# Performance work log

Hardware: AMD Instinct MI355X
Metric: run time of the kernel (lower is better)

The kernel has to match this reference:

```python
import jax, jax.numpy as jnp
import numpy as np
from jax import lax

E = 30      # embedding_dim
NH = 3      # attention heads
HD = E // NH
EPS = 1e-5


def _layer_norm(x, g, b):
    mu = jnp.mean(x, axis=-1, keepdims=True)
    var = jnp.mean(jnp.square(x - mu), axis=-1, keepdims=True)
    return (x - mu) * lax.rsqrt(var + EPS) * g + b


def setup_inputs() -> dict:
    key = jax.random.key(0)
    ks = jax.random.split(key, 16)
    B, T = 4096, 512
    s = 0.1  # param init scale
    return {
        "input": jax.random.normal(ks[0], (B, T, 5), jnp.float32),
        "w_ih": jax.random.normal(ks[1], (4 * E, 5), jnp.float32) * s,
        "w_hh": jax.random.normal(ks[2], (4 * E, E), jnp.float32) * s,
        "b_ih": jax.random.normal(ks[3], (4 * E,), jnp.float32) * s,
        "b_hh": jax.random.normal(ks[4], (4 * E,), jnp.float32) * s,
        "in_proj_w": jax.random.normal(ks[5], (3 * E, E), jnp.float32) * s,
        "in_proj_b": jax.random.normal(ks[6], (3 * E,), jnp.float32) * s,
        "out_proj_w": jax.random.normal(ks[7], (E, E), jnp.float32) * s,
        "out_proj_b": jax.random.normal(ks[8], (E,), jnp.float32) * s,
        "fc1_w": jax.random.normal(ks[9], (E, E), jnp.float32) * s,
        "fc1_b": jax.random.normal(ks[10], (E,), jnp.float32) * s,
        "fc2_w": jax.random.normal(ks[11], (E, E), jnp.float32) * s,
        "fc2_b": jax.random.normal(ks[12], (E,), jnp.float32) * s,
        "ln_g": jnp.ones((E,), jnp.float32),
        "ln_b": jnp.zeros((E,), jnp.float32),
        "out_w": jax.random.normal(ks[13], (3, E), jnp.float32) * s,
        "out_b": jax.random.normal(ks[14], (3,), jnp.float32) * s,
    }


def reference(input, w_ih, w_hh, b_ih, b_hh, in_proj_w, in_proj_b,
              out_proj_w, out_proj_b, fc1_w, fc1_b, fc2_w, fc2_b,
              ln_g, ln_b, out_w, out_b):
    B = input.shape[0]
    # --- LSTM (1 layer, batch_first); gate order i,f,g,o as in torch ---
    x_proj = jnp.einsum('bti,gi->btg', input, w_ih) + b_ih + b_hh  # [B,T,4E]

    def step(carry, xg):
        h, c = carry
        gates = xg + h @ w_hh.T
        i, f, g, o = jnp.split(gates, 4, axis=-1)
        i = jax.nn.sigmoid(i); f = jax.nn.sigmoid(f)
        g = jnp.tanh(g); o = jax.nn.sigmoid(o)
        c = f * c + i * g
        h = o * jnp.tanh(c)
        return (h, c), None

    h0 = jnp.zeros((B, E), input.dtype)
    (h_n, c_n), _ = lax.scan(step, (h0, h0), x_proj.transpose(1, 0, 2))

    # --- MultiheadAttention on 2D inputs: torch treats [B,E] as unbatched
    # sequences of length B, so attention mixes across the batch axis. ---
    q = h_n @ in_proj_w[:E].T + in_proj_b[:E]
    k = c_n @ in_proj_w[E:2 * E].T + in_proj_b[E:2 * E]
    v = c_n @ in_proj_w[2 * E:].T + in_proj_b[2 * E:]
    qh = q.reshape(B, NH, HD).transpose(1, 0, 2)  # [NH, B, HD]
    kh = k.reshape(B, NH, HD).transpose(1, 0, 2)
    vh = v.reshape(B, NH, HD).transpose(1, 0, 2)
    scores = jnp.einsum('hld,hmd->hlm', qh, kh) / np.sqrt(HD)  # [NH,B,B]
    attn = jax.nn.softmax(scores, axis=-1)
    ctx = jnp.einsum('hlm,hmd->hld', attn, vh)  # [NH,B,HD]
    attn_out = ctx.transpose(1, 0, 2).reshape(B, E) @ out_proj_w.T + out_proj_b

    # --- residual + shared LayerNorm + MLP (exact GELU) ---
    x1 = _layer_norm(attn_out + h_n, ln_g, ln_b)
    fc = jax.nn.gelu(x1 @ fc1_w.T + fc1_b, approximate=False) @ fc2_w.T + fc2_b
    x2 = _layer_norm(x1 + fc, ln_g, ln_b)
    return x2 @ out_w.T + out_b  # [B, 3]
```

## Files before the change

kernel.cpp:

```cpp
#include <hip/hip_runtime.h>
#include <math.h>

#define Bsz  4096
#define Tlen 512
#define NE   30
#define NIN  5
#define HD10 10
#define B10  (Bsz*HD10)

typedef _Float16 h2v  __attribute__((ext_vector_type(2)));
typedef _Float16 f16x8 __attribute__((ext_vector_type(8)));
typedef float    f32x4 __attribute__((ext_vector_type(4)));

__device__ __forceinline__ float fexp2(float x){ return __builtin_amdgcn_exp2f(x); }
__device__ __forceinline__ float frcp (float x){ return __builtin_amdgcn_rcpf(x); }
#define L2E 1.4426950408889634f

__device__ __forceinline__ void loadarr32(float arr[32], const float* bufrow){
  const float4* p4 = (const float4*)bufrow;
  #pragma unroll
  for (int q4=0;q4<8;q4++){ float4 vv=p4[q4]; arr[4*q4]=vv.x; arr[4*q4+1]=vv.y; arr[4*q4+2]=vv.z; arr[4*q4+3]=vv.w; }
}

#define XSTR 520

extern "C" __global__ void __launch_bounds__(512,1)
lstm_k(const float* __restrict__ input, const float* __restrict__ w_ih,
       const float* __restrict__ w_hh, const float* __restrict__ b_ih,
       const float* __restrict__ b_hh, const float* __restrict__ in_proj_w,
       const float* __restrict__ in_proj_b,
       float* __restrict__ qo, float* __restrict__ ko, float* __restrict__ vo,
       float* __restrict__ ho)
{
  __shared__ __align__(16) _Float16 hb[2*640];
  __shared__ __align__(16) _Float16 xh[16*XSTR];
  const int tid  = threadIdx.x;
  const int wv   = __builtin_amdgcn_readfirstlane(tid >> 6);
  const int lane = tid & 63;
  const int n    = lane & 15;
  const int quad = lane >> 4;
  const int b0   = blockIdx.x * 16;

  f16x8 ah, ax;
  f32x4 bi;
  {
    const int r  = n & 3;
    const int qm = n >> 2;
    const int dA = 8*qm + wv;
    const float sG = (r==2) ? (-2.f*L2E) : (-L2E);
    const bool rv = (dA < NE);
    const int grow = rv ? (r*NE + dA) : 0;
    #pragma unroll
    for (int j=0;j<8;++j){
      const int k = quad*8 + j;
      ah[j] = (rv && k < NE) ? (_Float16)(sG*w_hh[grow*NE + k]) : (_Float16)0;
      ax[j] = (rv && quad==0 && j < NIN) ? (_Float16)(sG*w_ih[grow*NIN + j]) : (_Float16)0;
    }
    const int d = 8*quad + wv;
    #pragma unroll
    for (int rr=0;rr<4;++rr){
      const float sR = (rr==2) ? (-2.f*L2E) : (-L2E);
      bi[rr] = (d < NE) ? sR*(b_ih[rr*NE+d] + b_hh[rr*NE+d]) : 0.f;
    }
  }
  for (int i=tid; i<640; i+=512) ((float*)hb)[i] = 0.f;
  for (int i=tid; i<16*XSTR; i+=512) xh[i] = (_Float16)0;
  __syncthreads();

  float cc=0.f, hh=0.f;
  const int rdo  = n*40 + 8*quad;
  const int wro  = n*40 + 8*quad + wv;
  const int xoff = n*XSTR;
  f16x8 xB;
  f32x4 Cx, Cy;

#define LSTM_STEP(CIN, COUT, RB, WB, TT2) do{ \
    const f16x8 bh_ = *(const f16x8*)(hb + (RB) + rdo); \
    COUT = __builtin_amdgcn_mfma_f32_16x16x32_f16(ax, xB, bi, 0,0,0); \
    xB = *(const f16x8*)(xh + xoff + ((TT2)&63)*8); \
    f32x4 C_ = __builtin_amdgcn_mfma_f32_16x16x32_f16(ah, bh_, CIN, 0,0,0); \
     \
    const float ei=fexp2(C_[0]), ef=fexp2(C_[1]); \
    const float eg=fexp2(C_[2]), eo=fexp2(C_[3]); \
    const float Af=1.f+ef, Bi_=1.f+ei, G2=1.f+eg; \
    cc = cc*frcp(Af) + (2.f-G2)*frcp(Bi_*G2); \
    const float e2=fexp2((2.f*L2E)*cc); \
    const float E2=1.f+e2; \
    hh = (E2-2.f)*frcp((1.f+eo)*E2); \
    hb[(WB) + wro] = (_Float16)hh; \
    __syncthreads(); \
  }while(0)

  for (int tc = 0; tc < Tlen; tc += 64) {
    for (int i4 = tid; i4 < 1280; i4 += 512){
      const int nn = i4/80, e4 = i4%80;
      const float4 v4 = *(const float4*)(input + (size_t)(b0+nn)*(Tlen*NIN) + tc*NIN + e4*4);
      #pragma unroll
      for (int u=0;u<4;++u){
        const int e = e4*4+u;
        xh[nn*XSTR + (e/5)*8 + (e%5)] = (_Float16)((&v4.x)[u]);
      }
    }
    __syncthreads();
    {
      const f16x8 x0 = *(const f16x8*)(xh + xoff);
      Cx = __builtin_amdgcn_mfma_f32_16x16x32_f16(ax, x0, bi, 0,0,0);
      xB = *(const f16x8*)(xh + xoff + 8);
    }
    #pragma unroll 1
    for (int tl = 0; tl < 64; tl += 2) {
      LSTM_STEP(Cx, Cy, 0,   640, tl+2);
      LSTM_STEP(Cy, Cx, 640, 0,   tl+3);
    }
  }
#undef LSTM_STEP

  float* hf = (float*)xh;
  float* cf = hf + 16*36;
  {
    hf[n*36 + 8*quad + wv] = hh;
    cf[n*36 + 8*quad + wv] = cc;
  }
  __syncthreads();
  for (int i = tid; i < 16*NE; i += 512){
    const int nn = i/NE, d = i%NE;
    ho[(size_t)(b0+nn)*NE + d] = hf[nn*36 + d];
  }
  const float QS = 0.31622776601683794f;
  for (int i = tid; i < 90*16; i += 512){
    const int o  = i % 90;
    const int nn = i / 90;
    const float* wrow = in_proj_w + o*NE;
    const float* src  = (o < NE) ? &hf[nn*36] : &cf[nn*36];
    float acc = in_proj_b[o];
    #pragma unroll
    for (int k2=0;k2<NE;k2++) acc = fmaf(wrow[k2], src[k2], acc);
    const int b = b0 + nn;
    if (o < 30)      { qo[(o/10)*B10 + b*10 + (o%10)] = acc * QS; }
    else if (o < 60) { const int u=o-30; ko[(u/10)*B10 + b*10 + (u%10)] = acc; }
    else             { const int u=o-60; vo[(u/10)*B10 + b*10 + (u%10)] = acc; }
  }
}

extern "C" __global__ void __launch_bounds__(256)
attn_part(const float* __restrict__ q, const float* __restrict__ k,
          const float* __restrict__ v, float* __restrict__ part, int nkeys)
{
  __shared__ __align__(16) float kst[640];
  __shared__ __align__(16) float vst[640];
  const int t    = threadIdx.x;
  const int qr   = blockIdx.x*256 + t;
  const int head = blockIdx.y;
  const int ks   = blockIdx.z;
  const float* kh = k + (size_t)head*B10;
  const float* vh = v + (size_t)head*B10;
  float qreg[10];
  {
    const float2* qp = (const float2*)(q + (size_t)head*B10 + (size_t)qr*10);
    #pragma unroll
    for (int i=0;i<5;i++){ float2 t2=qp[i]; qreg[2*i]=t2.x; qreg[2*i+1]=t2.y; }
  }
  float m = -INFINITY, l = 0.f, acc[10];
  #pragma unroll
  for (int d=0;d<10;d++) acc[d]=0.f;

  const int k0 = ks * nkeys;
  const int nt = nkeys >> 6;
  #pragma unroll 1
  for (int ti=0; ti<nt; ++ti){
    const int kt0 = k0 + (ti<<6);
    __syncthreads();
    {
      const float4* ksrc = (const float4*)(kh + (size_t)kt0*10);
      const float4* vsrc = (const float4*)(vh + (size_t)kt0*10);
      for (int i=t; i<320; i+=256){
        if (i < 160) ((float4*)kst)[i]     = ksrc[i];
        else         ((float4*)vst)[i-160] = vsrc[i-160];
      }
    }
    __syncthreads();
    #pragma unroll 1
    for (int c8=0; c8<64; c8+=8){
      float s[8];
      #pragma unroll
      for (int u=0;u<8;u++){
        const float2* kp = (const float2*)(kst + (c8+u)*10);
        float sv = 0.f;
        #pragma unroll
        for (int i=0;i<5;i++){ float2 kk=kp[i]; sv=fmaf(qreg[2*i],kk.x,sv); sv=fmaf(qreg[2*i+1],kk.y,sv); }
        s[u]=sv;
      }
      float mc = s[0];
      #pragma unroll
      for (int u=1;u<8;u++) mc = fmaxf(mc, s[u]);
      const float mnew = fmaxf(m, mc);
      const float corr = fexp2(L2E*(m - mnew));
      l *= corr;
      #pragma unroll
      for (int d=0;d<10;d++) acc[d]*=corr;
      #pragma unroll
      for (int u=0;u<8;u++){
        const float p = fexp2(L2E*(s[u]-mnew));
        l += p;
        const float2* vp = (const float2*)(vst + (c8+u)*10);
        #pragma unroll
        for (int i=0;i<5;i++){ float2 vv=vp[i]; acc[2*i]=fmaf(p,vv.x,acc[2*i]); acc[2*i+1]=fmaf(p,vv.y,acc[2*i+1]); }
      }
      m = mnew;
    }
  }
  float* pp = part + ((size_t)(head*Bsz + qr)*gridDim.z + ks)*12;
  pp[0]=m; pp[1]=l;
  #pragma unroll
  for (int d=0;d<10;d++) pp[2+d]=acc[d];
}

extern "C" __global__ void __launch_bounds__(256)
tail_k(const float* __restrict__ part, int ns, const float* __restrict__ hn,
       const float* __restrict__ out_proj_w, const float* __restrict__ out_proj_b,
       const float* __restrict__ fc1_w, const float* __restrict__ fc1_b,
       const float* __restrict__ fc2_w, const float* __restrict__ fc2_b,
       const float* __restrict__ ln_g, const float* __restrict__ ln_b,
       const float* __restrict__ out_w, const float* __restrict__ out_b,
       float* __restrict__ out)
{
  __shared__ __align__(16) float buf[4][32];
  __shared__ float wl[2880];
  const int tidb = threadIdx.x;
  for (int i=tidb;i<900;i+=256) wl[i]       = out_proj_w[i];
  for (int i=tidb;i<900;i+=256) wl[900+i]   = fc1_w[i];
  for (int i=tidb;i<900;i+=256) wl[1800+i]  = fc2_w[i];
  if (tidb < 90) wl[2700+tidb] = out_w[tidb];
  const int wave = tidb >> 6;
  const int lane = tidb & 63;
  const int b = blockIdx.x*4 + wave;
  const bool act = (lane < NE);
  if (lane < 32) buf[wave][lane] = 0.f;
  __syncthreads();
  if (act) {
    const int head = lane/10, dd = lane%10;
    const float* p = part + ((size_t)(head*Bsz + b)*ns)*12;
    float M = -INFINITY, L = 0.f, O = 0.f;
    for (int i=0;i<ns;i++){
      const float mi = p[i*12], li = p[i*12+1], ai = p[i*12+2+dd];
      const float Mn = fmaxf(M, mi);
      const float cw = fexp2(L2E*(M - Mn));
      const float wi = fexp2(L2E*(mi - Mn));
      L = fmaf(li, wi, L*cw);
      O = fmaf(ai, wi, O*cw);
      M = Mn;
    }
    buf[wave][lane] = O / L;
  }
  __builtin_amdgcn_wave_barrier();
  float arr[32];
  loadarr32(arr, &buf[wave][0]);
  const float hv = act ? hn[b*NE+lane] : 0.f;
  float x = 0.f;
  if (act) {
    float a = out_proj_b[lane];
    #pragma unroll
    for (int k2=0;k2<NE;k2++) a = fmaf(wl[lane*NE+k2], arr[k2], a);
    x = a + hv;
  }
  __builtin_amdgcn_wave_barrier();
  if (act) buf[wave][lane] = x;
  __builtin_amdgcn_wave_barrier();
  loadarr32(arr, &buf[wave][0]);
  float s1=0.f, s2=0.f;
  #pragma unroll
  for (int k2=0;k2<32;k2++){ s1+=arr[k2]; s2=fmaf(arr[k2],arr[k2],s2); }
  float mu = s1*(1.f/30.f);
  float var = s2*(1.f/30.f) - mu*mu;
  float rs = rsqrtf(var + 1e-5f);
  float x1 = 0.f;
  if (act) x1 = fmaf((x-mu)*rs, ln_g[lane], ln_b[lane]);
  __builtin_amdgcn_wave_barrier();
  if (act) buf[wave][lane] = x1;
  __builtin_amdgcn_wave_barrier();
  loadarr32(arr, &buf[wave][0]);
  float gv = 0.f;
  if (act) {
    float a = fc1_b[lane];
    #pragma unroll
    for (int k2=0;k2<NE;k2++) a = fmaf(wl[900+lane*NE+k2], arr[k2], a);
    gv = 0.5f*a*(1.f + erff(a*0.70710678118654752f));
  }
  __builtin_amdgcn_wave_barrier();
  if (act) buf[wave][lane] = gv;
  __builtin_amdgcn_wave_barrier();
  loadarr32(arr, &buf[wave][0]);
  float y = 0.f;
  if (act) {
    float a = fc2_b[lane];
    #pragma unroll
    for (int k2=0;k2<NE;k2++) a = fmaf(wl[1800+lane*NE+k2], arr[k2], a);
    y = x1 + a;
  }
  __builtin_amdgcn_wave_barrier();
  if (act) buf[wave][lane] = y;
  __builtin_amdgcn_wave_barrier();
  loadarr32(arr, &buf[wave][0]);
  s1=0.f; s2=0.f;
  #pragma unroll
  for (int k2=0;k2<32;k2++){ s1+=arr[k2]; s2=fmaf(arr[k2],arr[k2],s2); }
  mu = s1*(1.f/30.f);
  var = s2*(1.f/30.f) - mu*mu;
  rs = rsqrtf(var + 1e-5f);
  float x2 = 0.f;
  if (act) x2 = fmaf((y-mu)*rs, ln_g[lane], ln_b[lane]);
  __builtin_amdgcn_wave_barrier();
  if (act) buf[wave][lane] = x2;
  __builtin_amdgcn_wave_barrier();
  loadarr32(arr, &buf[wave][0]);
  if (lane < 3) {
    float a = out_b[lane];
    #pragma unroll
    for (int k2=0;k2<NE;k2++) a = fmaf(wl[2700+lane*NE+k2], arr[k2], a);
    out[b*3 + lane] = a;
  }
}

extern "C" void kernel_launch(void* const* d_in, const int* in_sizes, int n_in,
                              void* d_out, int out_size, void* d_ws, size_t ws_size,
                              hipStream_t stream)
{
  const float* input      = (const float*)d_in[0];
  const float* w_ih       = (const float*)d_in[1];
  const float* w_hh       = (const float*)d_in[2];
  const float* b_ih       = (const float*)d_in[3];
  const float* b_hh       = (const float*)d_in[4];
  const float* in_proj_w  = (const float*)d_in[5];
  const float* in_proj_b  = (const float*)d_in[6];
  const float* out_proj_w = (const float*)d_in[7];
  const float* out_proj_b = (const float*)d_in[8];
  const float* fc1_w      = (const float*)d_in[9];
  const float* fc1_b      = (const float*)d_in[10];
  const float* fc2_w      = (const float*)d_in[11];
  const float* fc2_b      = (const float*)d_in[12];
  const float* ln_g       = (const float*)d_in[13];
  const float* ln_b       = (const float*)d_in[14];
  const float* out_w      = (const float*)d_in[15];
  const float* out_b      = (const float*)d_in[16];

  float* ws = (float*)d_ws;
  float* qo   = ws;
  float* ko   = ws + 122880;
  float* vo   = ws + 245760;
  float* hn   = ws + 368640;
  float* part = ws + 491520;

  const size_t need16 = ((size_t)491520 + (size_t)3*4096*16*12) * 4;
  const int NS = (ws_size >= need16) ? 16 : 8;

  lstm_k<<<Bsz/16, 512, 0, stream>>>(input, w_ih, w_hh, b_ih, b_hh,
                                     in_proj_w, in_proj_b, qo, ko, vo, hn);
  attn_part<<<dim3(Bsz/256, 3, NS), 256, 0, stream>>>(qo, ko, vo, part, Bsz/NS);
  tail_k<<<Bsz/4, 256, 0, stream>>>(part, NS, hn, out_proj_w, out_proj_b,
                                    fc1_w, fc1_b, fc2_w, fc2_b,
                                    ln_g, ln_b, out_w, out_b, (float*)d_out);
}
```

Baseline: 289.4 us.

## Double-buffer K/V tiles in attention, vectorize LDS reads, raise key split

The attention partial kernel now double-buffers its K/V shared-memory tiles, prefetching the next 64-key tile while computing on the current one, which removes one barrier per tile. It also reads K/V rows as float4 pairs, folds the exp2 scaling into an fma, and writes the partial results with float4 stores. The host raises the key-split count to 32 when the workspace is large enough, giving more blocks for occupancy at the cost of more partials for the tail kernel to merge. Overall runtime is likely dominated by the LSTM kernel, so the attention gain may be small.

After: 288.5 us. No clear change (-0.3%).

```diff
diff --git a/kernel.cpp b/kernel.cpp
--- a/kernel.cpp
+++ b/kernel.cpp
@@ -146,8 +146,8 @@
 attn_part(const float* __restrict__ q, const float* __restrict__ k,
           const float* __restrict__ v, float* __restrict__ part, int nkeys)
 {
-  __shared__ __align__(16) float kst[640];
-  __shared__ __align__(16) float vst[640];
+  __shared__ __align__(16) float kst[2][640];
+  __shared__ __align__(16) float vst[2][640];
   const int t    = threadIdx.x;
   const int qr   = blockIdx.x*256 + t;
   const int head = blockIdx.y;
@@ -166,53 +166,81 @@
 
   const int k0 = ks * nkeys;
   const int nt = nkeys >> 6;
+  {
+    const float4* ksrc = (const float4*)(kh + (size_t)k0*10);
+    const float4* vsrc = (const float4*)(vh + (size_t)k0*10);
+    for (int i=t; i<320; i+=256){
+      if (i < 160) ((float4*)kst[0])[i]     = ksrc[i];
+      else         ((float4*)vst[0])[i-160] = vsrc[i-160];
+    }
+  }
   #pragma unroll 1
   for (int ti=0; ti<nt; ++ti){
-    const int kt0 = k0 + (ti<<6);
     __syncthreads();
-    {
-      const float4* ksrc = (const float4*)(kh + (size_t)kt0*10);
-      const float4* vsrc = (const float4*)(vh + (size_t)kt0*10);
+    const int cur = ti & 1;
+    if (ti+1 < nt){
+      const int kt = k0 + ((ti+1)<<6);
+      const float4* ksrc = (const float4*)(kh + (size_t)kt*10);
+      const float4* vsrc = (const float4*)(vh + (size_t)kt*10);
       for (int i=t; i<320; i+=256){
-        if (i < 160) ((float4*)kst)[i]     = ksrc[i];
-        else         ((float4*)vst)[i-160] = vsrc[i-160];
+        if (i < 160) ((float4*)kst[cur^1])[i]     = ksrc[i];
+        else         ((float4*)vst[cur^1])[i-160] = vsrc[i-160];
       }
     }
-    __syncthreads();
+    const float* kb = kst[cur];
+    const float* vb = vst[cur];
     #pragma unroll 1
     for (int c8=0; c8<64; c8+=8){
       float s[8];
       #pragma unroll
-      for (int u=0;u<8;u++){
-        const float2* kp = (const float2*)(kst + (c8+u)*10);
-        float sv = 0.f;
-        #pragma unroll
-        for (int i=0;i<5;i++){ float2 kk=kp[i]; sv=fmaf(qreg[2*i],kk.x,sv); sv=fmaf(qreg[2*i+1],kk.y,sv); }
-        s[u]=sv;
+      for (int u2=0;u2<4;u2++){
+        const float4* kp = (const float4*)(kb + (c8+2*u2)*10);
+        const float4 A=kp[0], B4=kp[1], C4=kp[2], D4=kp[3], E4=kp[4];
+        float s0 = qreg[0]*A.x;
+        s0=fmaf(qreg[1],A.y,s0);  s0=fmaf(qreg[2],A.z,s0);  s0=fmaf(qreg[3],A.w,s0);
+        s0=fmaf(qreg[4],B4.x,s0); s0=fmaf(qreg[5],B4.y,s0); s0=fmaf(qreg[6],B4.z,s0);
+        s0=fmaf(qreg[7],B4.w,s0); s0=fmaf(qreg[8],C4.x,s0); s0=fmaf(qreg[9],C4.y,s0);
+        float s1 = qreg[0]*C4.z;
+        s1=fmaf(qreg[1],C4.w,s1); s1=fmaf(qreg[2],D4.x,s1); s1=fmaf(qreg[3],D4.y,s1);
+        s1=fmaf(qreg[4],D4.z,s1); s1=fmaf(qreg[5],D4.w,s1); s1=fmaf(qreg[6],E4.x,s1);
+        s1=fmaf(qreg[7],E4.y,s1); s1=fmaf(qreg[8],E4.z,s1); s1=fmaf(qreg[9],E4.w,s1);
+        s[2*u2]=s0; s[2*u2+1]=s1;
       }
-      float mc = s[0];
-      #pragma unroll
-      for (int u=1;u<8;u++) mc = fmaxf(mc, s[u]);
+      float mc = fmaxf(fmaxf(fmaxf(s[0],s[1]),fmaxf(s[2],s[3])),
+                       fmaxf(fmaxf(s[4],s[5]),fmaxf(s[6],s[7])));
       const float mnew = fmaxf(m, mc);
       const float corr = fexp2(L2E*(m - mnew));
       l *= corr;
       #pragma unroll
       for (int d=0;d<10;d++) acc[d]*=corr;
+      const float mB = L2E*mnew;
       #pragma unroll
-      for (int u=0;u<8;u++){
-        const float p = fexp2(L2E*(s[u]-mnew));
-        l += p;
-        const float2* vp = (const float2*)(vst + (c8+u)*10);
-        #pragma unroll
-        for (int i=0;i<5;i++){ float2 vv=vp[i]; acc[2*i]=fmaf(p,vv.x,acc[2*i]); acc[2*i+1]=fmaf(p,vv.y,acc[2*i+1]); }
+      for (int u2=0;u2<4;u2++){
+        const float p0 = fexp2(fmaf(s[2*u2],  L2E, -mB));
+        const float p1 = fexp2(fmaf(s[2*u2+1],L2E, -mB));
+        l += p0; l += p1;
+        const float4* vp = (const float4*)(vb + (c8+2*u2)*10);
+        const float4 A=vp[0], B4=vp[1], C4=vp[2], D4=vp[3], E4=vp[4];
+        acc[0]=fmaf(p0,A.x,acc[0]);  acc[1]=fmaf(p0,A.y,acc[1]);
+        acc[2]=fmaf(p0,A.z,acc[2]);  acc[3]=fmaf(p0,A.w,acc[3]);
+        acc[4]=fmaf(p0,B4.x,acc[4]); acc[5]=fmaf(p0,B4.y,acc[5]);
+        acc[6]=fmaf(p0,B4.z,acc[6]); acc[7]=fmaf(p0,B4.w,acc[7]);
+        acc[8]=fmaf(p0,C4.x,acc[8]); acc[9]=fmaf(p0,C4.y,acc[9]);
+        acc[0]=fmaf(p1,C4.z,acc[0]); acc[1]=fmaf(p1,C4.w,acc[1]);
+        acc[2]=fmaf(p1,D4.x,acc[2]); acc[3]=fmaf(p1,D4.y,acc[3]);
+        acc[4]=fmaf(p1,D4.z,acc[4]); acc[5]=fmaf(p1,D4.w,acc[5]);
+        acc[6]=fmaf(p1,E4.x,acc[6]); acc[7]=fmaf(p1,E4.y,acc[7]);
+        acc[8]=fmaf(p1,E4.z,acc[8]); acc[9]=fmaf(p1,E4.w,acc[9]);
       }
       m = mnew;
     }
   }
-  float* pp = part + ((size_t)(head*Bsz + qr)*gridDim.z + ks)*12;
-  pp[0]=m; pp[1]=l;
-  #pragma unroll
-  for (int d=0;d<10;d++) pp[2+d]=acc[d];
+  float4 w0,w1,w2;
+  w0.x=m;      w0.y=l;      w0.z=acc[0]; w0.w=acc[1];
+  w1.x=acc[2]; w1.y=acc[3]; w1.z=acc[4]; w1.w=acc[5];
+  w2.x=acc[6]; w2.y=acc[7]; w2.z=acc[8]; w2.w=acc[9];
+  float4* pp4 = (float4*)(part + ((size_t)(head*Bsz + qr)*gridDim.z + ks)*12);
+  pp4[0]=w0; pp4[1]=w1; pp4[2]=w2;
 }
 
 extern "C" __global__ void __launch_bounds__(256)
@@ -350,8 +378,9 @@
   float* hn   = ws + 368640;
   float* part = ws + 491520;
 
+  const size_t need32 = ((size_t)491520 + (size_t)3*4096*32*12) * 4;
   const size_t need16 = ((size_t)491520 + (size_t)3*4096*16*12) * 4;
-  const int NS = (ws_size >= need16) ? 16 : 8;
+  const int NS = (ws_size >= need32) ? 32 : (ws_size >= need16) ? 16 : 8;
 
   lstm_k<<<Bsz/16, 512, 0, stream>>>(input, w_ih, w_hh, b_ih, b_hh,
                                      in_proj_w, in_proj_b, qo, ko, vo, hn);
```
